# Optimization experiments

Measured on AMD Instinct MI355X. Metric: run time of the kernel, lower is better.

Reference implementation:

```python
import jax, jax.numpy as jnp
import numpy as np

DIMS = 1024
HEADS = 16
DEPTH = DIMS // HEADS


def setup_inputs() -> dict:
    key = jax.random.key(0)
    kq, kk, kv = jax.random.split(key, 3)
    B, S = 2, 2048
    q = jax.random.normal(kq, (B, S, DIMS), dtype=jnp.float32)
    k = jax.random.normal(kk, (B, S, DIMS), dtype=jnp.float32)
    v = jax.random.normal(kv, (B, S, DIMS), dtype=jnp.float32)
    return {"q": q, "k": k, "v": v}


def _split_heads(x):
    # [B, S, dims] -> [B, heads, S, depth]
    b, s, _ = x.shape
    return x.reshape(b, s, HEADS, DEPTH).transpose(0, 2, 1, 3)


def reference(q, k, v):
    b, s, _ = q.shape
    qh = _split_heads(q)  # [b, h, sq, d]
    kh = _split_heads(k)  # [b, h, sk, d]
    vh = _split_heads(v)  # [b, h, sk, d]
    # keras.layers.Attention default: UNSCALED dot-product scores
    scores = jnp.einsum("bhqd,bhkd->bhqk", qh, kh)
    weights = jax.nn.softmax(scores, axis=-1)
    out = jnp.einsum("bhqk,bhkd->bhqd", weights, vh)
    # merge heads: [b, h, sq, d] -> [b, sq, dims]
    out = out.transpose(0, 2, 1, 3).reshape(b, s, DIMS)
    return out
```

## Files before the change

### kernel.cpp

```cpp
#include <hip/hip_runtime.h>

#define SEQ 2048
#define HEADS 16
#define DEPTH 64
#define DIMS 1024
#define LOG2E 1.44269504088896340736f

typedef _Float16 f16x8 __attribute__((ext_vector_type(8)));
typedef _Float16 f16x4 __attribute__((ext_vector_type(4)));
typedef __fp16 fp16v2 __attribute__((ext_vector_type(2)));
typedef float f32x4 __attribute__((ext_vector_type(4)));

__device__ __forceinline__ f32x4 mfma16(f16x8 a, f16x8 b, f32x4 c) {
  return __builtin_amdgcn_mfma_f32_16x16x32_f16(a, b, c, 0, 0, 0);
}

#if __has_builtin(__builtin_amdgcn_exp2f)
#define EXP2(x) __builtin_amdgcn_exp2f(x)
#else
#define EXP2(x) exp2f(x)
#endif

#define GLOAD_LDS(g, l)                                                        \
  __builtin_amdgcn_global_load_lds(                                            \
      (const __attribute__((address_space(1))) unsigned int*)(g),              \
      (__attribute__((address_space(3))) unsigned int*)(l), 16, 0, 0)

__global__ __launch_bounds__(256) void prep_k(const float* __restrict__ k,
                                              _Float16* __restrict__ kh) {
  int t = blockIdx.x * 256 + threadIdx.x;
  size_t flat = (size_t)t * 8;
  int b = (int)(flat >> 21);
  int rem = (int)(flat & ((1u << 21) - 1));
  int s = rem >> 10;
  int c = rem & 1023;
  int h = c >> 6;
  int d = c & 63;
  float4 a0 = *(const float4*)(k + flat);
  float4 a1 = *(const float4*)(k + flat + 4);
  float f[8] = {a0.x, a0.y, a0.z, a0.w, a1.x, a1.y, a1.z, a1.w};
  f16x8 th;
  #pragma unroll
  for (int j = 0; j < 8; ++j) th[j] = (_Float16)f[j];
  size_t o = ((size_t)(b * HEADS + h) * SEQ + s) * DEPTH + d;
  *(f16x8*)(kh + o) = th;
}

__global__ __launch_bounds__(256) void prep_v(const float* __restrict__ v,
                                              _Float16* __restrict__ vt) {
  int t = blockIdx.x * 256 + threadIdx.x;
  int d = t & 63;
  int sg = (t >> 6) & 255;
  int bh = t >> 14;
  int b = bh >> 4, h = bh & 15;
  int s0 = sg * 8;
  const float* src = v + ((size_t)(b * SEQ + s0)) * DIMS + h * DEPTH + d;
  _Float16* dst = vt + ((size_t)bh * DEPTH + d) * SEQ + s0;
  f16x8 tv;
  #pragma unroll
  for (int i = 0; i < 8; ++i) tv[i] = (_Float16)src[(size_t)i * DIMS];
  *(f16x8*)dst = tv;
}

__global__ __launch_bounds__(256, 2) void attn_fwd(
    const float* __restrict__ q, const _Float16* __restrict__ kh,
    const _Float16* __restrict__ vt, float* __restrict__ out) {
  __shared__ _Float16 Kl[2][64 * 64];
  __shared__ _Float16 Vl[2][64 * 64];
  __shared__ _Float16 Pl[4][32 * 64];

  const int tid = threadIdx.x;
  const int w = tid >> 6;
  const int l = tid & 63;
  const int lg = l >> 4;
  const int lr = l & 15;

  const int bid = blockIdx.x;
  const int wg = (bid & 7) * 64 + (bid >> 3);
  const int qt = wg & 15;
  const int bh = wg >> 4;
  const int b = bh >> 4;
  const int h = bh & 15;

  const int qb = qt * 128 + w * 32;
  const int hoff = h * DEPTH;
  const size_t kvoff = (size_t)bh * SEQ * DEPTH;

  f16x8 qf[2][2];
  #pragma unroll
  for (int mt = 0; mt < 2; ++mt) {
    const float* gq =
        q + (size_t)(b * SEQ + qb + mt * 16 + lr) * DIMS + hoff + 8 * lg;
    #pragma unroll
    for (int c = 0; c < 2; ++c) {
      float4 a0 = *(const float4*)(gq + 32 * c);
      float4 a1 = *(const float4*)(gq + 32 * c + 4);
      float f[8] = {a0.x, a0.y, a0.z, a0.w, a1.x, a1.y, a1.z, a1.w};
      f16x8 t;
      #pragma unroll
      for (int j = 0; j < 8; ++j) t[j] = (_Float16)(f[j] * LOG2E);
      qf[mt][c] = t;
    }
  }

  const int srow = l >> 3;
  const int scol = ((l & 7) ^ srow) * 8;
  const _Float16* gk0 = kh + kvoff + (size_t)(16 * w + srow) * DEPTH + scol;
  const _Float16* gv0 = vt + kvoff + (size_t)(16 * w + srow) * SEQ + scol;
  _Float16* Pw = &Pl[w][0];

  f32x4 acc[2][4] = {};
  float mrow[2] = {-3e38f, -3e38f};
  float den[2] = {0.f, 0.f};

  const int x7 = lr & 7;
  int kch[2];
  #pragma unroll
  for (int c = 0; c < 2; ++c) kch[c] = ((4 * c + lg) ^ x7) * 8;

  auto stage = [&](int buf, int t) {
    const _Float16* gk = gk0 + (size_t)t * 64 * DEPTH;
    const _Float16* gv = gv0 + (size_t)t * 64;
    GLOAD_LDS(gk, &Kl[buf][(16 * w) * 64]);
    GLOAD_LDS(gk + 8 * DEPTH, &Kl[buf][(16 * w + 8) * 64]);
    GLOAD_LDS(gv, &Vl[buf][(16 * w) * 64]);
    GLOAD_LDS(gv + (size_t)8 * SEQ, &Vl[buf][(16 * w + 8) * 64]);
  };

  auto compute = [&](int buf) {
    f32x4 st[2][4] = {};
    __builtin_amdgcn_s_setprio(1);
    #pragma unroll
    for (int nt = 0; nt < 4; ++nt)
      #pragma unroll
      for (int c = 0; c < 2; ++c) {
        f16x8 kf = *(const f16x8*)&Kl[buf][(nt * 16 + lr) * 64 + kch[c]];
        st[0][nt] = mfma16(kf, qf[0][c], st[0][nt]);
        st[1][nt] = mfma16(kf, qf[1][c], st[1][nt]);
      }
    __builtin_amdgcn_s_setprio(0);

    #pragma unroll
    for (int mt = 0; mt < 2; ++mt) {
      float pmax = st[mt][0][0];
      #pragma unroll
      for (int nt = 0; nt < 4; ++nt)
        #pragma unroll
        for (int r = 0; r < 4; ++r) pmax = fmaxf(pmax, st[mt][nt][r]);
      pmax = fmaxf(pmax, __shfl_xor(pmax, 16));
      pmax = fmaxf(pmax, __shfl_xor(pmax, 32));
      if (!__all(pmax - mrow[mt] <= 8.0f)) {
        float mnew = fmaxf(mrow[mt], pmax);
        float sc = EXP2(mrow[mt] - mnew);
        mrow[mt] = mnew;
        den[mt] *= sc;
        #pragma unroll
        for (int r = 0; r < 4; ++r) {
          float scb = __shfl(sc, (l & 48) | (4 * lg + r));
          #pragma unroll
          for (int dt = 0; dt < 4; ++dt) acc[mt][dt][r] *= scb;
        }
      }
      float rs = 0.f;
      #pragma unroll
      for (int nt = 0; nt < 4; ++nt) {
        float p0 = EXP2(st[mt][nt][0] - mrow[mt]);
        float p1 = EXP2(st[mt][nt][1] - mrow[mt]);
        float p2 = EXP2(st[mt][nt][2] - mrow[mt]);
        float p3 = EXP2(st[mt][nt][3] - mrow[mt]);
        rs += (p0 + p1) + (p2 + p3);
        union { fp16v2 h2[2]; f16x4 h4; } pu;
        pu.h2[0] = __builtin_amdgcn_cvt_pkrtz(p0, p1);
        pu.h2[1] = __builtin_amdgcn_cvt_pkrtz(p2, p3);
        const int chunk = (2 * nt + (lg >> 1)) ^ x7;
        *(f16x4*)&Pw[(mt * 16 + lr) * 64 + chunk * 8 + (lg & 1) * 4] = pu.h4;
      }
      rs += __shfl_xor(rs, 16);
      rs += __shfl_xor(rs, 32);
      den[mt] += rs;
    }

    __builtin_amdgcn_s_setprio(1);
    #pragma unroll
    for (int ks = 0; ks < 2; ++ks) {
      f16x8 pf0 = *(const f16x8*)&Pw[(0 * 16 + lr) * 64 + kch[ks]];
      f16x8 pf1 = *(const f16x8*)&Pw[(1 * 16 + lr) * 64 + kch[ks]];
      #pragma unroll
      for (int dt = 0; dt < 4; ++dt) {
        f16x8 vf = *(const f16x8*)&Vl[buf][(dt * 16 + lr) * 64 + kch[ks]];
        acc[0][dt] = mfma16(pf0, vf, acc[0][dt]);
        acc[1][dt] = mfma16(pf1, vf, acc[1][dt]);
      }
    }
    __builtin_amdgcn_s_setprio(0);
  };

  stage(0, 0);
  __syncthreads();
  for (int kt = 0; kt < SEQ / 64; kt += 2) {
    stage(1, kt + 1);
    compute(0);
    __syncthreads();
    if (kt + 2 < SEQ / 64) stage(0, kt + 2);
    compute(1);
    __syncthreads();
  }

  #pragma unroll
  for (int mt = 0; mt < 2; ++mt) {
    float rden[4];
    #pragma unroll
    for (int r = 0; r < 4; ++r)
      rden[r] = 1.0f / __shfl(den[mt], (l & 48) | (4 * lg + r));
    #pragma unroll
    for (int dt = 0; dt < 4; ++dt)
      #pragma unroll
      for (int r = 0; r < 4; ++r) {
        const int row = qb + mt * 16 + 4 * lg + r;
        out[(size_t)(b * SEQ + row) * DIMS + hoff + dt * 16 + lr] =
            acc[mt][dt][r] * rden[r];
      }
  }
}

extern "C" void kernel_launch(void* const* d_in, const int* in_sizes, int n_in,
                              void* d_out, int out_size, void* d_ws, size_t ws_size,
                              hipStream_t stream) {
  const float* q = (const float*)d_in[0];
  const float* k = (const float*)d_in[1];
  const float* v = (const float*)d_in[2];
  float* out = (float*)d_out;

  const size_t tsz = (size_t)2 * HEADS * SEQ * DEPTH;
  _Float16* khf = (_Float16*)d_ws;
  _Float16* vtp = khf + tsz;

  prep_k<<<2048, 256, 0, stream>>>(k, khf);
  prep_v<<<2048, 256, 0, stream>>>(v, vtp);
  attn_fwd<<<512, 256, 0, stream>>>(q, khf, vtp, out);
}
```

Measured before the change: 76.68 us.

## Load K tiles directly into registers and compute softmax denominator via MFMA

K tiles are now loaded from global memory straight into registers, double-buffered across iterations, instead of being staged through LDS. Each wave reads the full 64-row K tile itself, so global and L2 traffic for K goes up fourfold, but the K LDS buffers and their reads are gone. The softmax row sum is now accumulated by an extra MFMA against a ones vector using the fp16-rounded P values, replacing the per-lane sums and cross-lane shuffles. The row-max shuffle reduction now runs only inside the rare rescale branch. Keeping two K register sets adds register pressure at 2 blocks per CU.

```diff
diff --git a/kernel.cpp b/kernel.cpp
--- a/kernel.cpp
+++ b/kernel.cpp
@@ -65,7 +65,6 @@
 __global__ __launch_bounds__(256, 2) void attn_fwd(
     const float* __restrict__ q, const _Float16* __restrict__ kh,
     const _Float16* __restrict__ vt, float* __restrict__ out) {
-  __shared__ _Float16 Kl[2][64 * 64];
   __shared__ _Float16 Vl[2][64 * 64];
   __shared__ _Float16 Pl[4][32 * 64];
 
@@ -103,81 +102,88 @@
     }
   }
 
+  const _Float16* gkK = kh + kvoff + (size_t)lr * DEPTH + 8 * lg;
   const int srow = l >> 3;
   const int scol = ((l & 7) ^ srow) * 8;
-  const _Float16* gk0 = kh + kvoff + (size_t)(16 * w + srow) * DEPTH + scol;
   const _Float16* gv0 = vt + kvoff + (size_t)(16 * w + srow) * SEQ + scol;
   _Float16* Pw = &Pl[w][0];
 
   f32x4 acc[2][4] = {};
+  f32x4 dacc[2] = {};
   float mrow[2] = {-3e38f, -3e38f};
-  float den[2] = {0.f, 0.f};
 
   const int x7 = lr & 7;
   int kch[2];
   #pragma unroll
   for (int c = 0; c < 2; ++c) kch[c] = ((4 * c + lg) ^ x7) * 8;
 
-  auto stage = [&](int buf, int t) {
-    const _Float16* gk = gk0 + (size_t)t * 64 * DEPTH;
+  const f16x8 onesf = {1, 1, 1, 1, 1, 1, 1, 1};
+
+  auto kload = [&](int t, f16x8* dst) {
+    const _Float16* gk = gkK + (size_t)t * 64 * DEPTH;
+    #pragma unroll
+    for (int nt = 0; nt < 4; ++nt)
+      #pragma unroll
+      for (int c = 0; c < 2; ++c)
+        dst[nt * 2 + c] =
+            *(const f16x8*)(gk + (size_t)(nt * 16) * DEPTH + 32 * c);
+  };
+
+  auto stageV = [&](int buf, int t) {
     const _Float16* gv = gv0 + (size_t)t * 64;
-    GLOAD_LDS(gk, &Kl[buf][(16 * w) * 64]);
-    GLOAD_LDS(gk + 8 * DEPTH, &Kl[buf][(16 * w + 8) * 64]);
     GLOAD_LDS(gv, &Vl[buf][(16 * w) * 64]);
     GLOAD_LDS(gv + (size_t)8 * SEQ, &Vl[buf][(16 * w + 8) * 64]);
   };
 
-  auto compute = [&](int buf) {
+  auto compute = [&](int buf, f16x8* kf) {
     f32x4 st[2][4] = {};
     __builtin_amdgcn_s_setprio(1);
     #pragma unroll
     for (int nt = 0; nt < 4; ++nt)
       #pragma unroll
       for (int c = 0; c < 2; ++c) {
-        f16x8 kf = *(const f16x8*)&Kl[buf][(nt * 16 + lr) * 64 + kch[c]];
-        st[0][nt] = mfma16(kf, qf[0][c], st[0][nt]);
-        st[1][nt] = mfma16(kf, qf[1][c], st[1][nt]);
+        st[0][nt] = mfma16(kf[nt * 2 + c], qf[0][c], st[0][nt]);
+        st[1][nt] = mfma16(kf[nt * 2 + c], qf[1][c], st[1][nt]);
       }
     __builtin_amdgcn_s_setprio(0);
 
     #pragma unroll
     for (int mt = 0; mt < 2; ++mt) {
-      float pmax = st[mt][0][0];
-      #pragma unroll
-      for (int nt = 0; nt < 4; ++nt)
-        #pragma unroll
-        for (int r = 0; r < 4; ++r) pmax = fmaxf(pmax, st[mt][nt][r]);
-      pmax = fmaxf(pmax, __shfl_xor(pmax, 16));
-      pmax = fmaxf(pmax, __shfl_xor(pmax, 32));
+      float m0 = fmaxf(fmaxf(st[mt][0][0], st[mt][0][1]),
+                       fmaxf(st[mt][0][2], st[mt][0][3]));
+      float m1 = fmaxf(fmaxf(st[mt][1][0], st[mt][1][1]),
+                       fmaxf(st[mt][1][2], st[mt][1][3]));
+      float m2 = fmaxf(fmaxf(st[mt][2][0], st[mt][2][1]),
+                       fmaxf(st[mt][2][2], st[mt][2][3]));
+      float m3 = fmaxf(fmaxf(st[mt][3][0], st[mt][3][1]),
+                       fmaxf(st[mt][3][2], st[mt][3][3]));
+      float pmax = fmaxf(fmaxf(m0, m1), fmaxf(m2, m3));
       if (!__all(pmax - mrow[mt] <= 8.0f)) {
+        pmax = fmaxf(pmax, __shfl_xor(pmax, 16));
+        pmax = fmaxf(pmax, __shfl_xor(pmax, 32));
         float mnew = fmaxf(mrow[mt], pmax);
         float sc = EXP2(mrow[mt] - mnew);
         mrow[mt] = mnew;
-        den[mt] *= sc;
         #pragma unroll
         for (int r = 0; r < 4; ++r) {
           float scb = __shfl(sc, (l & 48) | (4 * lg + r));
+          dacc[mt][r] *= scb;
           #pragma unroll
           for (int dt = 0; dt < 4; ++dt) acc[mt][dt][r] *= scb;
         }
       }
-      float rs = 0.f;
       #pragma unroll
       for (int nt = 0; nt < 4; ++nt) {
         float p0 = EXP2(st[mt][nt][0] - mrow[mt]);
         float p1 = EXP2(st[mt][nt][1] - mrow[mt]);
         float p2 = EXP2(st[mt][nt][2] - mrow[mt]);
         float p3 = EXP2(st[mt][nt][3] - mrow[mt]);
-        rs += (p0 + p1) + (p2 + p3);
         union { fp16v2 h2[2]; f16x4 h4; } pu;
         pu.h2[0] = __builtin_amdgcn_cvt_pkrtz(p0, p1);
         pu.h2[1] = __builtin_amdgcn_cvt_pkrtz(p2, p3);
         const int chunk = (2 * nt + (lg >> 1)) ^ x7;
         *(f16x4*)&Pw[(mt * 16 + lr) * 64 + chunk * 8 + (lg & 1) * 4] = pu.h4;
       }
-      rs += __shfl_xor(rs, 16);
-      rs += __shfl_xor(rs, 32);
-      den[mt] += rs;
     }
 
     __builtin_amdgcn_s_setprio(1);
@@ -185,6 +191,8 @@
     for (int ks = 0; ks < 2; ++ks) {
       f16x8 pf0 = *(const f16x8*)&Pw[(0 * 16 + lr) * 64 + kch[ks]];
       f16x8 pf1 = *(const f16x8*)&Pw[(1 * 16 + lr) * 64 + kch[ks]];
+      dacc[0] = mfma16(pf0, onesf, dacc[0]);
+      dacc[1] = mfma16(pf1, onesf, dacc[1]);
       #pragma unroll
       for (int dt = 0; dt < 4; ++dt) {
         f16x8 vf = *(const f16x8*)&Vl[buf][(dt * 16 + lr) * 64 + kch[ks]];
@@ -195,23 +203,28 @@
     __builtin_amdgcn_s_setprio(0);
   };
 
-  stage(0, 0);
+  f16x8 kA[8], kB[8];
+  kload(0, kA);
+  stageV(0, 0);
   __syncthreads();
   for (int kt = 0; kt < SEQ / 64; kt += 2) {
-    stage(1, kt + 1);
-    compute(0);
+    stageV(1, kt + 1);
+    kload(kt + 1, kB);
+    compute(0, kA);
     __syncthreads();
-    if (kt + 2 < SEQ / 64) stage(0, kt + 2);
-    compute(1);
+    if (kt + 2 < SEQ / 64) {
+      stageV(0, kt + 2);
+      kload(kt + 2, kA);
+    }
+    compute(1, kB);
     __syncthreads();
   }
 
   #pragma unroll
   for (int mt = 0; mt < 2; ++mt) {
-    float rden[4];
-    #pragma unroll
-    for (int r = 0; r < 4; ++r)
-      rden[r] = 1.0f / __shfl(den[mt], (l & 48) | (4 * lg + r));
+    f32x4 rden;
+    #pragma unroll
+    for (int r = 0; r < 4; ++r) rden[r] = 1.0f / dacc[mt][r];
     #pragma unroll
     for (int dt = 0; dt < 4; ++dt)
       #pragma unroll
```

Result: slower. 87.35 us (+13.9%).
